# Performance work log

Hardware: AMD Instinct MI355X
Metric: run time of the kernel (lower is better)

Reference implementation:

```python
import jax, jax.numpy as jnp
import numpy as np
import math

CHUNK = 64

def _linear(x, W, b):
    # torch nn.Linear: y = x @ W.T + b
    return jnp.einsum('bsd,ed->bse', x, W) + b

def setup_inputs() -> dict:
    key = jax.random.key(0)
    ks = jax.random.split(key, 10)
    B, S, D = 4, 4096, 512
    scale = 0.02
    inp = {
        'x': jax.random.normal(ks[0], (B, S, D), jnp.float32),
        'base_phases': jax.random.normal(ks[1], (S, D), jnp.float32) * math.pi,
        'Wk': jax.random.normal(ks[2], (D, D), jnp.float32) * scale,
        'bk': jnp.zeros((D,), jnp.float32),
        'Wv': jax.random.normal(ks[3], (D, D), jnp.float32) * scale,
        'bv': jnp.zeros((D,), jnp.float32),
        'Wq': jax.random.normal(ks[4], (D, D), jnp.float32) * scale,
        'bq': jnp.zeros((D,), jnp.float32),
        'Wkm': jax.random.normal(ks[5], (D, D), jnp.float32) * scale,
        'bkm': jnp.zeros((D,), jnp.float32),
        'Wqm': jax.random.normal(ks[6], (D, D), jnp.float32) * scale,
        'bqm': jnp.zeros((D,), jnp.float32),
        'mod_scale': jnp.ones((1,), jnp.float32) * 0.1,
        'ln_g': jnp.ones((D,), jnp.float32),
        'ln_b': jnp.zeros((D,), jnp.float32),
        'Wo': jax.random.normal(ks[7], (D, D), jnp.float32) * scale,
        'bo': jnp.zeros((D,), jnp.float32),
    }
    return inp

def reference(x, base_phases, Wk, bk, Wv, bv, Wq, bq, Wkm, bkm, Wqm, bqm, mod_scale, ln_g, ln_b, Wo, bo):
    B, S, D = x.shape
    bp = base_phases[:S][None]                      # [1,S,D]
    key = _linear(x, Wk, bk)
    value = _linear(x, Wv, bv)
    query = _linear(x, Wq, bq)
    key_phase = bp + _linear(key, Wkm, bkm) * mod_scale
    query_phase = bp + _linear(query, Wqm, bqm) * mod_scale
    bound_real = value * jnp.cos(key_phase)
    bound_imag = value * jnp.sin(key_phase)
    # chunked cumulative memory (S divisible by CHUNK -> no padding)
    nC = S // CHUNK
    br = bound_real.reshape(B, nC, CHUNK, D)
    bi = bound_imag.reshape(B, nC, CHUNK, D)
    qp = query_phase.reshape(B, nC, CHUNK, D)
    mem_real = jnp.cumsum(br, axis=2)
    mem_imag = jnp.cumsum(bi, axis=2)
    retrieved = (mem_real * jnp.cos(qp) + mem_imag * jnp.sin(qp)).reshape(B, S, D)
    retrieved = retrieved / math.sqrt(D)
    # LayerNorm + Linear (to_out)
    mu = jnp.mean(retrieved, axis=-1, keepdims=True)
    var = jnp.mean((retrieved - mu) ** 2, axis=-1, keepdims=True)
    normed = (retrieved - mu) / jnp.sqrt(var + 1e-5) * ln_g + ln_b
    out = _linear(normed, Wo, bo)
    return x + out
```

## Files before the change

### kernel.cpp

```cpp
#include <hip/hip_runtime.h>
#include <hip/hip_bf16.h>


typedef __attribute__((ext_vector_type(8))) short short8;
typedef __attribute__((ext_vector_type(4))) float f32x4;

#define M_TOK   16384
#define DIM     512
#define NCHUNK  64
#define RPAD    520

__device__ __forceinline__ void gll16(const void* g, void* l) {
  __builtin_amdgcn_global_load_lds(
      (const __attribute__((address_space(1))) unsigned int*)g,
      (__attribute__((address_space(3))) unsigned int*)l, 16, 0, 0);
}

__device__ __forceinline__ uint2 pack4bf(float4 v) {
  union { __hip_bfloat16 h[4]; uint2 u; } t;
  t.h[0] = __float2bfloat16(v.x);
  t.h[1] = __float2bfloat16(v.y);
  t.h[2] = __float2bfloat16(v.z);
  t.h[3] = __float2bfloat16(v.w);
  return t.u;
}

__global__ __launch_bounds__(256) void prep_all(
    const float* __restrict__ x, __hip_bfloat16* __restrict__ x_bf,
    const float* __restrict__ Wv, const float* __restrict__ Wo,
    const float* __restrict__ bv,
    const float* __restrict__ Wkm, const float* __restrict__ Wqm,
    const float* __restrict__ Wk, const float* __restrict__ Wq,
    const float* __restrict__ bk, const float* __restrict__ bkm,
    const float* __restrict__ bq, const float* __restrict__ bqm,
    __hip_bfloat16* __restrict__ Wall, float* __restrict__ bc1,
    __hip_bfloat16* __restrict__ Wm_bf, __hip_bfloat16* __restrict__ WT_bf) {
  const int tid = threadIdx.x;
  if (blockIdx.x < 8192) {
    int i = blockIdx.x * 256 + tid;
    ((uint2*)x_bf)[i] = pack4bf(((const float4*)x)[i]);
    return;
  }
  const int b = blockIdx.x - 8192;
  if (b < 512) {
    int m = b >> 8;
    int idx = ((b & 255) * 256 + tid) * 4;
    const float* src = m ? Wo : Wv;
    __hip_bfloat16* dst = Wall + (m ? (size_t)1536 * 512 : 0);
    ((uint2*)dst)[idx >> 2] = pack4bf(*(const float4*)(src + idx));
    int t = b * 256 + tid;
    if (t < 512) bc1[t] = bv[t];
  } else if (b < 1024) {
    int bb = b - 512;
    int m = bb >> 8;
    int idx = ((bb & 255) * 256 + tid) * 4;
    const float* src = m ? Wqm : Wkm;
    ((uint2*)(Wm_bf + (size_t)m * 262144))[idx >> 2] =
        pack4bf(*(const float4*)(src + idx));
  } else if (b < 1152) {
    __shared__ float tile[64][65];
    int bb = b - 1024;
    int z = bb >> 6;
    int tl = bb & 63;
    int tr = tl >> 3, tc = tl & 7;
    const float* src = z ? Wq : Wk;
#pragma unroll
    for (int i = 0; i < 4; i++) {
      int r = (tid >> 4) + 16 * i;
      int c4 = (tid & 15) * 4;
      float4 v = *(const float4*)(src + (size_t)(tr * 64 + r) * 512 +
                                  tc * 64 + c4);
      tile[r][c4 + 0] = v.x;
      tile[r][c4 + 1] = v.y;
      tile[r][c4 + 2] = v.z;
      tile[r][c4 + 3] = v.w;
    }
    __syncthreads();
    int orow = tid >> 2;
    int seg = tid & 3;
    __hip_bfloat16* dst = WT_bf + (size_t)z * 262144 +
                          (size_t)(tc * 64 + orow) * 512 + tr * 64 + seg * 16;
#pragma unroll
    for (int q = 0; q < 4; q++) {
      float4 v;
      v.x = tile[seg * 16 + q * 4 + 0][orow];
      v.y = tile[seg * 16 + q * 4 + 1][orow];
      v.z = tile[seg * 16 + q * 4 + 2][orow];
      v.w = tile[seg * 16 + q * 4 + 3][orow];
      *(uint2*)(dst + q * 4) = pack4bf(v);
    }
  } else {
    int row = (b - 1152) * 4 + (tid >> 6);
    int lane = tid & 63;
    int z = row >> 9;
    int i = row & 511;
    const float* Wm = z ? Wqm : Wkm;
    const float* b0 = z ? bq : bk;
    const float* bm = z ? bqm : bkm;
    const float4* w4 = (const float4*)(Wm + (size_t)i * 512 + lane * 8);
    const float4* v4 = (const float4*)(b0 + lane * 8);
    float4 w0 = w4[0], w1 = w4[1], c0 = v4[0], c1 = v4[1];
    float acc = w0.x * c0.x + w0.y * c0.y + w0.z * c0.z + w0.w * c0.w +
                w1.x * c1.x + w1.y * c1.y + w1.z * c1.z + w1.w * c1.w;
#pragma unroll
    for (int off = 32; off; off >>= 1) acc += __shfl_xor(acc, off, 64);
    if (lane == 0) bc1[512 + z * 512 + i] = acc + bm[i];
  }
}

__global__ __launch_bounds__(256) void gemm_bt(
    const __hip_bfloat16* __restrict__ A, int lda,
    const __hip_bfloat16* __restrict__ Bt,
    const float* __restrict__ bias,
    __hip_bfloat16* __restrict__ Cout, int ldc) {
  constexpr int K = 512, BK = 32;
  __shared__ __align__(16) __hip_bfloat16 As[2][128 * BK];
  __shared__ __align__(16) __hip_bfloat16 Bs[2][128 * BK];

  const int tid  = threadIdx.x;
  const int lane = tid & 63;
  const int w    = tid >> 6;
  const int wm   = w >> 1;
  const int wn   = w & 1;
  const int lb = (blockIdx.x & 7) * 192 + (blockIdx.x >> 3);
  const int by = lb / 12;
  const int bx = lb - by * 12;
  const int m0 = by * 128;
  const int n0 = bx * 128;

  const int rS0    = (w * 2 + 0) * 16 + (lane >> 2);
  const int rS1    = (w * 2 + 1) * 16 + (lane >> 2);
  const int kInRow = (lane & 3) * 8;
  const __hip_bfloat16* gA0 = A + (size_t)(m0 + rS0) * lda + kInRow;
  const __hip_bfloat16* gA1 = A + (size_t)(m0 + rS1) * lda + kInRow;
  const __hip_bfloat16* gB0 = Bt + (size_t)(n0 + rS0) * K + kInRow;
  const __hip_bfloat16* gB1 = Bt + (size_t)(n0 + rS1) * K + kInRow;
  char* ldsA0 = (char*)&As[0][0] + (w * 2 + 0) * 1024;
  char* ldsA1 = (char*)&As[0][0] + (w * 2 + 1) * 1024;
  char* ldsB0 = (char*)&Bs[0][0] + (w * 2 + 0) * 1024;
  char* ldsB1 = (char*)&Bs[0][0] + (w * 2 + 1) * 1024;

  f32x4 acc[4][4] = {};

  const int rfA = lane & 15;
  const int rfK = (lane >> 4) * 8;

  gll16(gA0, ldsA0);
  gll16(gA1, ldsA1);
  gll16(gB0, ldsB0);
  gll16(gB1, ldsB1);

#pragma unroll 2
  for (int kt = 0; kt < K; kt += BK) {
    const int cur = (kt >> 5) & 1;
    const int coff = cur * 8192;
    __syncthreads();
    const int nxt = kt + BK;
    if (nxt < K) {
      const int noff = 8192 - coff;
      gll16(gA0 + nxt, ldsA0 + noff);
      gll16(gA1 + nxt, ldsA1 + noff);
      gll16(gB0 + nxt, ldsB0 + noff);
      gll16(gB1 + nxt, ldsB1 + noff);
    }
    const __hip_bfloat16* Ah = &As[cur][0];
    const __hip_bfloat16* Bh = &Bs[cur][0];
    short8 af[4], bfv[4];
#pragma unroll
    for (int i = 0; i < 4; i++)
      af[i] = *(const short8*)(Ah + (wm * 64 + i * 16 + rfA) * BK + rfK);
#pragma unroll
    for (int j = 0; j < 4; j++)
      bfv[j] = *(const short8*)(Bh + (wn * 64 + j * 16 + rfA) * BK + rfK);
#pragma unroll
    for (int i = 0; i < 4; i++)
#pragma unroll
      for (int j = 0; j < 4; j++)
        acc[i][j] = __builtin_amdgcn_mfma_f32_16x16x32_bf16(
            af[i], bfv[j], acc[i][j], 0, 0, 0);
  }

  const int cq = lane >> 4;
#pragma unroll
  for (int i = 0; i < 4; i++) {
    int row = m0 + wm * 64 + i * 16 + cq * 4;
#pragma unroll
    for (int j = 0; j < 4; j++) {
      int col = n0 + wn * 64 + j * 16 + (lane & 15);
      float bz = bias[col];
#pragma unroll
      for (int r = 0; r < 4; r++) {
        float v = acc[i][j][r] + bz;
        Cout[(size_t)(row + r) * ldc + col] = __float2bfloat16(v);
      }
    }
  }
}

__global__ __launch_bounds__(256) void gemm_compose(
    const __hip_bfloat16* __restrict__ Wm_bf,
    const __hip_bfloat16* __restrict__ WT_bf,
    __hip_bfloat16* __restrict__ Wall) {
  constexpr int K = 512, BK = 32;
  const __hip_bfloat16* A  = Wm_bf + (size_t)blockIdx.z * 262144;
  const __hip_bfloat16* Bt = WT_bf + (size_t)blockIdx.z * 262144;
  __hip_bfloat16* C = Wall + (size_t)(512 + blockIdx.z * 512) * 512;
  __shared__ __align__(16) __hip_bfloat16 As[128 * BK];
  __shared__ __align__(16) __hip_bfloat16 Bs[128 * BK];

  const int tid  = threadIdx.x;
  const int lane = tid & 63;
  const int w    = tid >> 6;
  const int wm   = w >> 1;
  const int wn   = w & 1;
  const int m0   = blockIdx.y * 128;
  const int n0   = blockIdx.x * 128;

  const int rS0    = (w * 2 + 0) * 16 + (lane >> 2);
  const int rS1    = (w * 2 + 1) * 16 + (lane >> 2);
  const int kInRow = (lane & 3) * 8;
  const __hip_bfloat16* gA0 = A + (size_t)(m0 + rS0) * K + kInRow;
  const __hip_bfloat16* gA1 = A + (size_t)(m0 + rS1) * K + kInRow;
  const __hip_bfloat16* gB0 = Bt + (size_t)(n0 + rS0) * K + kInRow;
  const __hip_bfloat16* gB1 = Bt + (size_t)(n0 + rS1) * K + kInRow;
  char* ldsA0 = (char*)As + (w * 2 + 0) * 1024;
  char* ldsA1 = (char*)As + (w * 2 + 1) * 1024;
  char* ldsB0 = (char*)Bs + (w * 2 + 0) * 1024;
  char* ldsB1 = (char*)Bs + (w * 2 + 1) * 1024;

  f32x4 acc[4][4] = {};
  const int rfA = lane & 15;
  const int rfK = (lane >> 4) * 8;

  for (int kt = 0; kt < K; kt += BK) {
    __syncthreads();
    gll16(gA0 + kt, ldsA0);
    gll16(gA1 + kt, ldsA1);
    gll16(gB0 + kt, ldsB0);
    gll16(gB1 + kt, ldsB1);
    __syncthreads();

    short8 af[4], bf[4];
#pragma unroll
    for (int i = 0; i < 4; i++)
      af[i] = *(const short8*)(As + (wm * 64 + i * 16 + rfA) * BK + rfK);
#pragma unroll
    for (int j = 0; j < 4; j++)
      bf[j] = *(const short8*)(Bs + (wn * 64 + j * 16 + rfA) * BK + rfK);
#pragma unroll
    for (int i = 0; i < 4; i++)
#pragma unroll
      for (int j = 0; j < 4; j++)
        acc[i][j] = __builtin_amdgcn_mfma_f32_16x16x32_bf16(
            af[i], bf[j], acc[i][j], 0, 0, 0);
  }

  const int cq = lane >> 4;
#pragma unroll
  for (int i = 0; i < 4; i++) {
    int row = m0 + wm * 64 + i * 16 + cq * 4;
#pragma unroll
    for (int j = 0; j < 4; j++) {
      int col = n0 + wn * 64 + j * 16 + (lane & 15);
#pragma unroll
      for (int r = 0; r < 4; r++)
        C[(size_t)(row + r) * 512 + col] = __float2bfloat16(acc[i][j][r]);
    }
  }
}

__global__ __launch_bounds__(1024) void fused_pg(
    const __hip_bfloat16* __restrict__ VKQ,
    const float* __restrict__ bp,
    const float* __restrict__ mod_scale,
    const float* __restrict__ ln_g, const float* __restrict__ ln_b,
    const __hip_bfloat16* __restrict__ WoB,
    const float* __restrict__ bo,
    const float* __restrict__ x,
    float* __restrict__ out) {
  __shared__ __hip_bfloat16 R[64 * RPAD];
  __shared__ float Tr[512], Ti[512];
  const int tid    = threadIdx.x;
  const int seg    = tid >> 9;
  const int d      = tid & 511;
  const int blk    = blockIdx.x;
  const int token0 = blk * 64;
  const int sg0    = (blk & (NCHUNK - 1)) * 64;
  const float msc  = mod_scale[0];
  const float isd  = 0.044194173824159216f;

  {
    const int s0 = seg * 32;
    float mr = 0.f, mi = 0.f;
    const __hip_bfloat16* vb = VKQ + (size_t)(token0 + s0) * 1536 + d;
    const float* bb = bp + (size_t)(sg0 + s0) * 512 + d;
#pragma unroll 4
    for (int s = 0; s < 32; ++s) {
      float v  = __bfloat162float(vb[(size_t)s * 1536]);
      float km = __bfloat162float(vb[(size_t)s * 1536 + 512]);
      float qm = __bfloat162float(vb[(size_t)s * 1536 + 1024]);
      float b  = bb[(size_t)s * 512];
      float kp = b + km * msc;
      float qp = b + qm * msc;
      float sk, ck, sq, cq;
      __sincosf(kp, &sk, &ck);
      __sincosf(qp, &sq, &cq);
      mr += v * ck;
      mi += v * sk;
      R[(s0 + s) * RPAD + d] = __float2bfloat16((mr * cq + mi * sq) * isd);
    }
    if (seg == 0) {
      Tr[d] = mr;
      Ti[d] = mi;
    }
  }
  __syncthreads();

  {
    const int r0 = 32 + seg * 16;
    const float pr = Tr[d] * isd;
    const float pi = Ti[d] * isd;
    const __hip_bfloat16* qb = VKQ + (size_t)(token0 + r0) * 1536 + 1024 + d;
    const float* bb = bp + (size_t)(sg0 + r0) * 512 + d;
#pragma unroll 4
    for (int s = 0; s < 16; ++s) {
      float qm = __bfloat162float(qb[(size_t)s * 1536]);
      float b  = bb[(size_t)s * 512];
      float qp = b + qm * msc;
      float sq, cq;
      __sincosf(qp, &sq, &cq);
      int idx = (r0 + s) * RPAD + d;
      float v = __bfloat162float(R[idx]) + pr * cq + pi * sq;
      R[idx] = __float2bfloat16(v);
    }
  }
  __syncthreads();

  {
    const int lane = tid & 63;
    const int wv   = tid >> 6;
    float gj[8], bj[8];
#pragma unroll
    for (int j = 0; j < 8; j++) {
      int col = lane + 64 * j;
      gj[j] = ln_g[col];
      bj[j] = ln_b[col];
    }
    for (int rr = 0; rr < 4; ++rr) {
      int row = wv * 4 + rr;
      float vals[8], sum = 0.f, sq2 = 0.f;
#pragma unroll
      for (int j = 0; j < 8; j++) {
        float v = __bfloat162float(R[row * RPAD + lane + 64 * j]);
        vals[j] = v;
        sum += v;
        sq2 += v * v;
      }
#pragma unroll
      for (int off = 32; off; off >>= 1) {
        sum += __shfl_xor(sum, off, 64);
        sq2 += __shfl_xor(sq2, off, 64);
      }
      float mu   = sum * (1.f / 512.f);
      float var  = sq2 * (1.f / 512.f) - mu * mu;
      float rstd = rsqrtf(var + 1e-5f);
#pragma unroll
      for (int j = 0; j < 8; j++) {
        float nv = (vals[j] - mu) * rstd * gj[j] + bj[j];
        R[row * RPAD + lane + 64 * j] = __float2bfloat16(nv);
      }
    }
  }
  __syncthreads();

  {
    const int lane = tid & 63;
    const int w    = tid >> 6;
    const int rfA  = lane & 15;
    const int rfK  = (lane >> 4) * 8;
    f32x4 acc[4][2] = {};

    for (int kt = 0; kt < 512; kt += 32) {
      short8 af[4], bf[2];
#pragma unroll
      for (int j = 0; j < 2; j++) {
        int col = w * 32 + j * 16 + rfA;
        bf[j] = *(const short8*)(WoB + (size_t)col * 512 + kt + rfK);
      }
#pragma unroll
      for (int i = 0; i < 4; i++)
        af[i] = *(const short8*)(R + (i * 16 + rfA) * RPAD + kt + rfK);
#pragma unroll
      for (int i = 0; i < 4; i++)
#pragma unroll
        for (int j = 0; j < 2; j++)
          acc[i][j] = __builtin_amdgcn_mfma_f32_16x16x32_bf16(
              af[i], bf[j], acc[i][j], 0, 0, 0);
    }

    const int cq = lane >> 4;
    float bz[2];
#pragma unroll
    for (int j = 0; j < 2; j++) bz[j] = bo[w * 32 + j * 16 + (lane & 15)];
#pragma unroll
    for (int i = 0; i < 4; i++) {
      int row = token0 + i * 16 + cq * 4;
#pragma unroll
      for (int j = 0; j < 2; j++) {
        int col = w * 32 + j * 16 + (lane & 15);
#pragma unroll
        for (int r = 0; r < 4; r++) {
          size_t o = (size_t)(row + r) * 512 + col;
          out[o] = acc[i][j][r] + bz[j] + x[o];
        }
      }
    }
  }
}

extern "C" void kernel_launch(void* const* d_in, const int* in_sizes, int n_in,
                              void* d_out, int out_size, void* d_ws,
                              size_t ws_size, hipStream_t stream) {
  const float* x    = (const float*)d_in[0];
  const float* bp   = (const float*)d_in[1];
  const float* Wk   = (const float*)d_in[2];
  const float* bk   = (const float*)d_in[3];
  const float* Wv   = (const float*)d_in[4];
  const float* bv   = (const float*)d_in[5];
  const float* Wq   = (const float*)d_in[6];
  const float* bq   = (const float*)d_in[7];
  const float* Wkm  = (const float*)d_in[8];
  const float* bkm  = (const float*)d_in[9];
  const float* Wqm  = (const float*)d_in[10];
  const float* bqm  = (const float*)d_in[11];
  const float* msc  = (const float*)d_in[12];
  const float* lng  = (const float*)d_in[13];
  const float* lnb  = (const float*)d_in[14];
  const float* Wo   = (const float*)d_in[15];
  const float* bo   = (const float*)d_in[16];
  float* out = (float*)d_out;

  char* ws = (char*)d_ws;
  __hip_bfloat16* x_bf  = (__hip_bfloat16*)ws;  ws += (size_t)M_TOK * DIM * 2;
  __hip_bfloat16* Wall  = (__hip_bfloat16*)ws;  ws += (size_t)2048 * 512 * 2;
  __hip_bfloat16* Wm_bf = (__hip_bfloat16*)ws;  ws += (size_t)2 * 262144 * 2;
  __hip_bfloat16* WT_bf = (__hip_bfloat16*)ws;  ws += (size_t)2 * 262144 * 2;
  float*          bc1   = (float*)ws;           ws += 1536 * 4;
  __hip_bfloat16* VKQ   = (__hip_bfloat16*)ws;  ws += (size_t)M_TOK * 1536 * 2;

  prep_all<<<9600, 256, 0, stream>>>(x, x_bf, Wv, Wo, bv, Wkm, Wqm, Wk, Wq,
                                     bk, bkm, bq, bqm, Wall, bc1, Wm_bf,
                                     WT_bf);
  gemm_compose<<<dim3(4, 4, 2), 256, 0, stream>>>(Wm_bf, WT_bf, Wall);
  gemm_bt<<<dim3(1536), 256, 0, stream>>>(x_bf, DIM, Wall, bc1, VKQ, 1536);
  fused_pg<<<256, 1024, 0, stream>>>(VKQ, bp, msc, lng, lnb,
                                     Wall + (size_t)1536 * 512, bo, x, out);
}
```

Baseline: 206.6 us.

## Prefetch two K-tiles ahead in GEMM with explicit waitcnt and MFMA priority

```diff
diff --git a/kernel.cpp b/kernel.cpp
--- a/kernel.cpp
+++ b/kernel.cpp
@@ -108,6 +108,34 @@
   }
 }
 
+#define GTILE(BUF, T, STAGE_EN, WN)                                         \
+  {                                                                         \
+    asm volatile("s_waitcnt vmcnt(" WN ")" ::: "memory");                   \
+    __builtin_amdgcn_s_barrier();                                           \
+    short8 af[4], bfv[4];                                                   \
+    _Pragma("unroll") for (int i = 0; i < 4; i++)                           \
+      af[i] = *(const short8*)(&As[BUF][0] +                                \
+                               (wm * 64 + i * 16 + rfA) * BK + rfK);        \
+    _Pragma("unroll") for (int j = 0; j < 4; j++)                           \
+      bfv[j] = *(const short8*)(&Bs[BUF][0] +                               \
+                                (wn * 64 + j * 16 + rfA) * BK + rfK);       \
+    if (STAGE_EN) {                                                         \
+      asm volatile("s_waitcnt lgkmcnt(0)" ::: "memory");                    \
+      __builtin_amdgcn_s_barrier();                                         \
+      const int nk = ((T) + 2) * BK;                                        \
+      gll16(gA0 + nk, ldsA0 + (BUF) * 8192);                                \
+      gll16(gA1 + nk, ldsA1 + (BUF) * 8192);                                \
+      gll16(gB0 + nk, ldsB0 + (BUF) * 8192);                                \
+      gll16(gB1 + nk, ldsB1 + (BUF) * 8192);                                \
+    }                                                                       \
+    __builtin_amdgcn_s_setprio(1);                                          \
+    _Pragma("unroll") for (int i = 0; i < 4; i++)                           \
+      _Pragma("unroll") for (int j = 0; j < 4; j++)                         \
+        acc[i][j] = __builtin_amdgcn_mfma_f32_16x16x32_bf16(                \
+            af[i], bfv[j], acc[i][j], 0, 0, 0);                             \
+    __builtin_amdgcn_s_setprio(0);                                          \
+  }
+
 __global__ __launch_bounds__(256) void gemm_bt(
     const __hip_bfloat16* __restrict__ A, int lda,
     const __hip_bfloat16* __restrict__ Bt,
@@ -149,36 +177,18 @@
   gll16(gA1, ldsA1);
   gll16(gB0, ldsB0);
   gll16(gB1, ldsB1);
-
-#pragma unroll 2
-  for (int kt = 0; kt < K; kt += BK) {
-    const int cur = (kt >> 5) & 1;
-    const int coff = cur * 8192;
-    __syncthreads();
-    const int nxt = kt + BK;
-    if (nxt < K) {
-      const int noff = 8192 - coff;
-      gll16(gA0 + nxt, ldsA0 + noff);
-      gll16(gA1 + nxt, ldsA1 + noff);
-      gll16(gB0 + nxt, ldsB0 + noff);
-      gll16(gB1 + nxt, ldsB1 + noff);
-    }
-    const __hip_bfloat16* Ah = &As[cur][0];
-    const __hip_bfloat16* Bh = &Bs[cur][0];
-    short8 af[4], bfv[4];
-#pragma unroll
-    for (int i = 0; i < 4; i++)
-      af[i] = *(const short8*)(Ah + (wm * 64 + i * 16 + rfA) * BK + rfK);
-#pragma unroll
-    for (int j = 0; j < 4; j++)
-      bfv[j] = *(const short8*)(Bh + (wn * 64 + j * 16 + rfA) * BK + rfK);
-#pragma unroll
-    for (int i = 0; i < 4; i++)
-#pragma unroll
-      for (int j = 0; j < 4; j++)
-        acc[i][j] = __builtin_amdgcn_mfma_f32_16x16x32_bf16(
-            af[i], bfv[j], acc[i][j], 0, 0, 0);
-  }
+  gll16(gA0 + BK, ldsA0 + 8192);
+  gll16(gA1 + BK, ldsA1 + 8192);
+  gll16(gB0 + BK, ldsB0 + 8192);
+  gll16(gB1 + BK, ldsB1 + 8192);
+
+#pragma unroll
+  for (int t = 0; t < 14; t += 2) {
+    GTILE(0, t, 1, "4");
+    GTILE(1, t + 1, 1, "4");
+  }
+  GTILE(0, 14, 0, "4");
+  GTILE(1, 15, 0, "0");
 
   const int cq = lane >> 4;
 #pragma unroll
```

Result: faster. 201.9 us (-2.2%).
